# Optimization experiments

Measured on AMD Instinct MI355X. Metric: run time of the kernel, lower is better.

## Reference

```python
import jax, jax.numpy as jnp
import numpy as np

N, L, D = 32768, 15, 256
VOCAB, SCORE_MAX = 27, 100


def setup_inputs() -> dict:
    key = jax.random.key(0)
    ks = jax.random.split(key, 16)
    inp = {
        'words': jax.random.randint(ks[0], (N, L), 0, VOCAB, dtype=jnp.int32),
        'rows': jax.random.randint(ks[1], (N,), 0, L, dtype=jnp.int32),
        'cols': jax.random.randint(ks[2], (N,), 0, L, dtype=jnp.int32),
        'dirs': jax.random.randint(ks[3], (N,), 0, 2, dtype=jnp.int32),
        'scores': jax.random.randint(ks[4], (N,), 0, 150, dtype=jnp.int32),
        'letter_emb': jax.random.normal(ks[5], (VOCAB, D), jnp.float32),
        'positional': jax.random.normal(ks[6], (L, D), jnp.float32),
        'Wq': jax.random.normal(ks[7], (D, D), jnp.float32) / np.sqrt(D),
        'bq': jax.random.normal(ks[8], (D,), jnp.float32) * 0.01,
        'Wk': jax.random.normal(ks[9], (D, D), jnp.float32) / np.sqrt(D),
        'bk': jax.random.normal(ks[10], (D,), jnp.float32) * 0.01,
        'Wv': jax.random.normal(ks[11], (D, D), jnp.float32) / np.sqrt(D),
        'bv': jax.random.normal(ks[12], (D,), jnp.float32) * 0.01,
        'row_emb': jax.random.normal(ks[13], (L, D), jnp.float32),
        'col_emb': jax.random.normal(ks[14], (L, D), jnp.float32),
        'dir_emb': jax.random.normal(ks[15], (2, D), jnp.float32),
        'score_emb': jax.random.normal(jax.random.fold_in(key, 99), (SCORE_MAX, D), jnp.float32),
    }
    return inp


def reference(words, rows, cols, dirs, scores, letter_emb, positional, Wq, bq, Wk, bk, Wv, bv, row_emb, col_emb, dir_emb, score_emb):
    # WordEncoder: letter embedding + positional, then single-head self-attention, sum over positions
    emb = letter_emb[words] + positional[None, :, :]            # [N, L, D]
    q = emb @ Wq.T + bq                                          # [N, L, D]
    k = emb @ Wk.T + bk
    v = emb @ Wv.T + bv
    att = jax.nn.softmax(jnp.einsum('nld,nmd->nlm', q, k), axis=-1)  # [N, L, L]
    word = jnp.einsum('nlm,nmd->nd', att, v)                     # (att @ v).sum(axis=1) -> [N, D]
    # VectorEncoder
    vector = row_emb[rows] + col_emb[cols] + dir_emb[dirs]       # [N, D]
    # score embedding (clamped to score_max - 1)
    score_v = score_emb[jnp.minimum(scores, SCORE_MAX - 1)]      # [N, D]
    # original computes word_enc(move.word) twice (word + ordered) -> 2 * word
    return 2.0 * word + vector + score_v
```

## Files before the change

### kernel.cpp

```cpp
#include <hip/hip_runtime.h>
#include <hip/hip_bf16.h>

#define NMOV 32768
#define LW 15
#define DIM 256
#define NVOC 27
#define NR 405
#define GSH 408
#define MPB 8

__device__ __forceinline__ float b2f(unsigned short u) {
    return __uint_as_float(((unsigned int)u) << 16);
}

__device__ const unsigned char PAIR_LUT[120] = {
    0x00,
    0x10,0x11,
    0x20,0x21,0x22,
    0x30,0x31,0x32,0x33,
    0x40,0x41,0x42,0x43,0x44,
    0x50,0x51,0x52,0x53,0x54,0x55,
    0x60,0x61,0x62,0x63,0x64,0x65,0x66,
    0x70,0x71,0x72,0x73,0x74,0x75,0x76,0x77,
    0x80,0x81,0x82,0x83,0x84,0x85,0x86,0x87,0x88,
    0x90,0x91,0x92,0x93,0x94,0x95,0x96,0x97,0x98,0x99,
    0xA0,0xA1,0xA2,0xA3,0xA4,0xA5,0xA6,0xA7,0xA8,0xA9,0xAA,
    0xB0,0xB1,0xB2,0xB3,0xB4,0xB5,0xB6,0xB7,0xB8,0xB9,0xBA,0xBB,
    0xC0,0xC1,0xC2,0xC3,0xC4,0xC5,0xC6,0xC7,0xC8,0xC9,0xCA,0xCB,0xCC,
    0xD0,0xD1,0xD2,0xD3,0xD4,0xD5,0xD6,0xD7,0xD8,0xD9,0xDA,0xDB,0xDC,0xDD,
    0xE0,0xE1,0xE2,0xE3,0xE4,0xE5,0xE6,0xE7,0xE8,0xE9,0xEA,0xEB,0xEC,0xED,0xEE
};

__global__ __launch_bounds__(256) void qkv_tables(
    const float* __restrict__ le, const float* __restrict__ pos,
    const float* __restrict__ Wq, const float* __restrict__ bq,
    const float* __restrict__ Wk, const float* __restrict__ bk,
    const float* __restrict__ Wv, const float* __restrict__ bv,
    float* __restrict__ QT, float* __restrict__ KT,
    __hip_bfloat16* __restrict__ VT)
{
    const int b   = blockIdx.x;
    const int c   = b / 15;
    const int rem = b % 15;
    const int lg  = rem / 3;
    const int mat = rem % 3;
    const int d   = threadIdx.x;

    const float* W  = (mat == 0) ? Wq : (mat == 1) ? Wk : Wv;
    const float* bb = (mat == 0) ? bq : (mat == 1) ? bk : bv;

    __shared__ float e[3][DIM];
    const float lv = le[c * DIM + d];
    #pragma unroll
    for (int k = 0; k < 3; ++k)
        e[k][d] = lv + pos[(lg * 3 + k) * DIM + d];
    __syncthreads();

    float acc[3];
    const float bias = bb[d];
    #pragma unroll
    for (int k = 0; k < 3; ++k) acc[k] = bias;

    const float4* w4 = (const float4*)(W + d * DIM);
    #pragma unroll 8
    for (int j4 = 0; j4 < DIM / 4; ++j4) {
        float4 w = w4[j4];
        #pragma unroll
        for (int k = 0; k < 3; ++k) {
            float4 e4 = *(const float4*)&e[k][j4 * 4];
            acc[k] += e4.x * w.x + e4.y * w.y + e4.z * w.z + e4.w * w.w;
        }
    }
    #pragma unroll
    for (int k = 0; k < 3; ++k) {
        int r = c * LW + lg * 3 + k;
        if (mat == 0)      QT[r * DIM + d] = acc[k];
        else if (mat == 1) KT[r * DIM + d] = acc[k];
        else               VT[r * DIM + d] = __float2bfloat16(acc[k]);
    }
}

__global__ __launch_bounds__(256) void h_matrix(
    const float* __restrict__ QT, const float* __restrict__ KT,
    float2* __restrict__ H)
{
    __shared__ float Qi[16][68], Ki[16][68], Qj[16][68], Kj[16][68];

    int rem = blockIdx.x, bi = 0, cnt = 26;
    while (rem >= cnt) { rem -= cnt; ++bi; --cnt; }
    const int bj = bi + rem;
    const int i0 = bi * 16, j0 = bj * 16;
    const int t = threadIdx.x;
    const int ti = t >> 4, tj = t & 15;

    float acc_ij = 0.f, acc_ji = 0.f;

    for (int k0 = 0; k0 < DIM; k0 += 64) {
        #pragma unroll
        for (int s = 0; s < 4; ++s) {
            int slot = s * 256 + t;
            int tile = slot >> 8;
            int r    = (slot >> 4) & 15;
            int c4   = slot & 15;
            int grow = (tile < 2) ? (i0 + r) : (j0 + r);
            const float* src = (tile == 0 || tile == 2) ? QT : KT;
            float4 v = (grow < NR)
                ? *(const float4*)&src[grow * DIM + k0 + c4 * 4]
                : make_float4(0.f, 0.f, 0.f, 0.f);
            float* dst = (tile == 0) ? &Qi[r][c4 * 4]
                       : (tile == 1) ? &Ki[r][c4 * 4]
                       : (tile == 2) ? &Qj[r][c4 * 4] : &Kj[r][c4 * 4];
            *(float4*)dst = v;
        }
        __syncthreads();
        #pragma unroll 4
        for (int k = 0; k < 64; k += 4) {
            float4 qi = *(const float4*)&Qi[ti][k];
            float4 kj = *(const float4*)&Kj[tj][k];
            float4 qj = *(const float4*)&Qj[ti][k];
            float4 ki = *(const float4*)&Ki[tj][k];
            acc_ij += qi.x * kj.x + qi.y * kj.y + qi.z * kj.z + qi.w * kj.w;
            acc_ji += qj.x * ki.x + qj.y * ki.y + qj.z * ki.z + qj.w * ki.w;
        }
        __syncthreads();
    }

    Qi[ti][tj] = acc_ij;
    Ki[ti][tj] = acc_ji;
    __syncthreads();
    const float t_ij = Qi[tj][ti];
    const float t_ji = Ki[tj][ti];

    const int i1 = i0 + ti, j1 = j0 + tj;
    if (i1 < NR && j1 < NR) H[i1 * GSH + j1] = make_float2(acc_ij, t_ji);
    const int i2 = j0 + ti, j2 = i0 + tj;
    if (i2 < NR && j2 < NR) H[i2 * GSH + j2] = make_float2(acc_ji, t_ij);
}

__global__ __launch_bounds__(256) void moves_kernel(
    const int* __restrict__ words, const int* __restrict__ rowsI,
    const int* __restrict__ colsI, const int* __restrict__ dirsI,
    const int* __restrict__ scoresI,
    const float2* __restrict__ H, const __hip_bfloat16* __restrict__ VT,
    const float* __restrict__ row_emb, const float* __restrict__ col_emb,
    const float* __restrict__ dir_emb, const float* __restrict__ score_emb,
    float* __restrict__ out)
{
    __shared__ float S[MPB][LW][17];
    __shared__ int   rIdx[MPB][16];
    __shared__ float csum[MPB][16];
    const int base = blockIdx.x * MPB;
    const int t = threadIdx.x;
    const int mv = t >> 5;
    const int j  = t & 31;

    if (j < LW)
        rIdx[mv][j] = words[(base + mv) * LW + j] * LW + j;
    __builtin_amdgcn_wave_barrier();

    #pragma unroll
    for (int k = 0; k < 4; ++k) {
        int p = j + 32 * k;
        if (p < 120) {
            int lm = PAIR_LUT[p];
            int l = lm >> 4, m = lm & 15;
            int rl = rIdx[mv][l], rm = rIdx[mv][m];
            float2 hv = H[(size_t)rl * GSH + rm];
            S[mv][l][m] = hv.x;
            S[mv][m][l] = hv.y;
        }
    }
    __builtin_amdgcn_wave_barrier();

    if (j < LW) {
        float s[LW];
        #pragma unroll
        for (int m = 0; m < LW; ++m) s[m] = S[mv][j][m];
        float mx = s[0];
        #pragma unroll
        for (int m = 1; m < LW; ++m) mx = fmaxf(mx, s[m]);
        float sum = 0.f;
        #pragma unroll
        for (int m = 0; m < LW; ++m) { s[m] = __expf(s[m] - mx); sum += s[m]; }
        float inv = 1.0f / sum;
        #pragma unroll
        for (int m = 0; m < LW; ++m) S[mv][j][m] = s[m] * inv;
    }
    __builtin_amdgcn_wave_barrier();

    if (j < LW) {
        float acc = 0.f;
        #pragma unroll
        for (int l = 0; l < LW; ++l) acc += S[mv][l][j];
        csum[mv][j] = acc;
    }
    __builtin_amdgcn_wave_barrier();

    const int wv = t >> 6;
    const int d0 = (t & 63) * 4;
    #pragma unroll
    for (int s2 = 0; s2 < 2; ++s2) {
        const int i = wv * 2 + s2;
        const int n = base + i;
        float wx = 0.f, wy = 0.f, wz = 0.f, ww = 0.f;
        #pragma unroll
        for (int m = 0; m < LW; ++m) {
            float c = csum[i][m];
            int r = rIdx[i][m];
            ushort4 vv = *(const ushort4*)((const unsigned short*)VT + (size_t)r * DIM + d0);
            wx += c * b2f(vv.x); wy += c * b2f(vv.y);
            wz += c * b2f(vv.z); ww += c * b2f(vv.w);
        }
        float4 re = *(const float4*)&row_emb[rowsI[n] * DIM + d0];
        float4 ce = *(const float4*)&col_emb[colsI[n] * DIM + d0];
        float4 de = *(const float4*)&dir_emb[dirsI[n] * DIM + d0];
        float4 se = *(const float4*)&score_emb[min(scoresI[n], 99) * DIM + d0];
        float4 res;
        res.x = 2.f * wx + re.x + ce.x + de.x + se.x;
        res.y = 2.f * wy + re.y + ce.y + de.y + se.y;
        res.z = 2.f * wz + re.z + ce.z + de.z + se.z;
        res.w = 2.f * ww + re.w + ce.w + de.w + se.w;
        *(float4*)&out[(size_t)n * DIM + d0] = res;
    }
}

extern "C" void kernel_launch(void* const* d_in, const int* in_sizes, int n_in,
                              void* d_out, int out_size, void* d_ws, size_t ws_size,
                              hipStream_t stream)
{
    const int*   words      = (const int*)d_in[0];
    const int*   rowsI      = (const int*)d_in[1];
    const int*   colsI      = (const int*)d_in[2];
    const int*   dirsI      = (const int*)d_in[3];
    const int*   scoresI    = (const int*)d_in[4];
    const float* letter_emb = (const float*)d_in[5];
    const float* positional = (const float*)d_in[6];
    const float* Wq         = (const float*)d_in[7];
    const float* bq         = (const float*)d_in[8];
    const float* Wk         = (const float*)d_in[9];
    const float* bk         = (const float*)d_in[10];
    const float* Wv         = (const float*)d_in[11];
    const float* bv         = (const float*)d_in[12];
    const float* row_emb    = (const float*)d_in[13];
    const float* col_emb    = (const float*)d_in[14];
    const float* dir_emb    = (const float*)d_in[15];
    const float* score_emb  = (const float*)d_in[16];
    float* out = (float*)d_out;

    float*  QT = (float*)d_ws;
    float*  KT = QT + NR * DIM;
    float2* Hm = (float2*)(KT + NR * DIM);
    __hip_bfloat16* VT = (__hip_bfloat16*)((char*)Hm + (size_t)NR * GSH * sizeof(float2));

    qkv_tables<<<405, 256, 0, stream>>>(letter_emb, positional, Wq, bq, Wk, bk,
                                        Wv, bv, QT, KT, VT);
    h_matrix<<<351, 256, 0, stream>>>(QT, KT, Hm);
    moves_kernel<<<NMOV / MPB, 256, 0, stream>>>(words, rowsI, colsI, dirsI,
                                                 scoresI, Hm, VT, row_emb,
                                                 col_emb, dir_emb, score_emb,
                                                 out);
}
```

Measured before the change: 68.65 us.

## Tile QKV table GEMM in shared memory and prefetch V rows in moves kernel

```diff
diff --git a/kernel.cpp b/kernel.cpp
--- a/kernel.cpp
+++ b/kernel.cpp
@@ -31,7 +31,7 @@
     0xE0,0xE1,0xE2,0xE3,0xE4,0xE5,0xE6,0xE7,0xE8,0xE9,0xEA,0xEB,0xEC,0xED,0xEE
 };
 
-__global__ __launch_bounds__(256) void qkv_tables(
+__global__ __launch_bounds__(256) void qkv_gemm(
     const float* __restrict__ le, const float* __restrict__ pos,
     const float* __restrict__ Wq, const float* __restrict__ bq,
     const float* __restrict__ Wk, const float* __restrict__ bk,
@@ -39,44 +39,74 @@
     float* __restrict__ QT, float* __restrict__ KT,
     __hip_bfloat16* __restrict__ VT)
 {
-    const int b   = blockIdx.x;
-    const int c   = b / 15;
-    const int rem = b % 15;
-    const int lg  = rem / 3;
-    const int mat = rem % 3;
-    const int d   = threadIdx.x;
-
+    __shared__ float Ash[32][260];
+    __shared__ float Bsh[256][69];
+    const int t  = threadIdx.x;
+    const int gx = blockIdx.x % 12;
+    const int gy = blockIdx.x / 12;
+    const int r0 = gy * 32;
+    const int mat = gx >> 2;
+    const int nb  = (gx & 3) * 64;
     const float* W  = (mat == 0) ? Wq : (mat == 1) ? Wk : Wv;
     const float* bb = (mat == 0) ? bq : (mat == 1) ? bk : bv;
 
-    __shared__ float e[3][DIM];
-    const float lv = le[c * DIM + d];
-    #pragma unroll
-    for (int k = 0; k < 3; ++k)
-        e[k][d] = lv + pos[(lg * 3 + k) * DIM + d];
+    #pragma unroll
+    for (int s = 0; s < 8; ++s) {
+        int slot = s * 256 + t;
+        int row = slot >> 6, q4 = slot & 63;
+        int r = r0 + row;
+        float4 v = make_float4(0.f, 0.f, 0.f, 0.f);
+        if (r < NR) {
+            int c = r / 15, l = r - c * 15;
+            float4 lv = *(const float4*)&le[c * DIM + q4 * 4];
+            float4 pv = *(const float4*)&pos[l * DIM + q4 * 4];
+            v = make_float4(lv.x + pv.x, lv.y + pv.y, lv.z + pv.z, lv.w + pv.w);
+        }
+        *(float4*)&Ash[row][q4 * 4] = v;
+    }
+    #pragma unroll
+    for (int s = 0; s < 16; ++s) {
+        int slot = s * 256 + t;
+        int row = slot >> 6, q4 = slot & 63;
+        float4 w4 = *(const float4*)&W[(nb + row) * DIM + q4 * 4];
+        Bsh[q4 * 4 + 0][row] = w4.x;
+        Bsh[q4 * 4 + 1][row] = w4.y;
+        Bsh[q4 * 4 + 2][row] = w4.z;
+        Bsh[q4 * 4 + 3][row] = w4.w;
+    }
     __syncthreads();
 
-    float acc[3];
-    const float bias = bb[d];
-    #pragma unroll
-    for (int k = 0; k < 3; ++k) acc[k] = bias;
-
-    const float4* w4 = (const float4*)(W + d * DIM);
-    #pragma unroll 8
-    for (int j4 = 0; j4 < DIM / 4; ++j4) {
-        float4 w = w4[j4];
-        #pragma unroll
-        for (int k = 0; k < 3; ++k) {
-            float4 e4 = *(const float4*)&e[k][j4 * 4];
-            acc[k] += e4.x * w.x + e4.y * w.y + e4.z * w.z + e4.w * w.w;
-        }
-    }
-    #pragma unroll
-    for (int k = 0; k < 3; ++k) {
-        int r = c * LW + lg * 3 + k;
-        if (mat == 0)      QT[r * DIM + d] = acc[k];
-        else if (mat == 1) KT[r * DIM + d] = acc[k];
-        else               VT[r * DIM + d] = __float2bfloat16(acc[k]);
+    const int tn = t & 63, tm = t >> 6;
+    float acc[8];
+    #pragma unroll
+    for (int rr = 0; rr < 8; ++rr) acc[rr] = 0.f;
+
+    #pragma unroll 4
+    for (int kq = 0; kq < 64; ++kq) {
+        float4 a4[8];
+        #pragma unroll
+        for (int rr = 0; rr < 8; ++rr)
+            a4[rr] = *(const float4*)&Ash[tm * 8 + rr][kq * 4];
+        float b0 = Bsh[kq * 4 + 0][tn];
+        float b1 = Bsh[kq * 4 + 1][tn];
+        float b2 = Bsh[kq * 4 + 2][tn];
+        float b3 = Bsh[kq * 4 + 3][tn];
+        #pragma unroll
+        for (int rr = 0; rr < 8; ++rr)
+            acc[rr] += a4[rr].x * b0 + a4[rr].y * b1 + a4[rr].z * b2 + a4[rr].w * b3;
+    }
+
+    const float bias = bb[nb + tn];
+    const int dcol = nb + tn;
+    #pragma unroll
+    for (int rr = 0; rr < 8; ++rr) {
+        int r = r0 + tm * 8 + rr;
+        if (r < NR) {
+            float v = acc[rr] + bias;
+            if (mat == 0)      QT[r * DIM + dcol] = v;
+            else if (mat == 1) KT[r * DIM + dcol] = v;
+            else               VT[r * DIM + dcol] = __float2bfloat16(v);
+        }
     }
 }
 
@@ -158,16 +188,41 @@
         rIdx[mv][j] = words[(base + mv) * LW + j] * LW + j;
     __builtin_amdgcn_wave_barrier();
 
+    const int wv = t >> 6;
+    const int d0 = (t & 63) * 4;
+    const unsigned short* VT16 = (const unsigned short*)VT;
+
+    float2 hv[4];
+    int ll[4], mm[4];
     #pragma unroll
     for (int k = 0; k < 4; ++k) {
         int p = j + 32 * k;
         if (p < 120) {
             int lm = PAIR_LUT[p];
-            int l = lm >> 4, m = lm & 15;
-            int rl = rIdx[mv][l], rm = rIdx[mv][m];
-            float2 hv = H[(size_t)rl * GSH + rm];
-            S[mv][l][m] = hv.x;
-            S[mv][m][l] = hv.y;
+            ll[k] = lm >> 4; mm[k] = lm & 15;
+            int rl = rIdx[mv][ll[k]], rm = rIdx[mv][mm[k]];
+            hv[k] = H[(size_t)rl * GSH + rm];
+        }
+    }
+
+    const int iA = wv * 2, nA = base + iA;
+    ushort4 vvA[LW];
+    #pragma unroll
+    for (int m = 0; m < LW; ++m) {
+        int r = rIdx[iA][m];
+        vvA[m] = *(const ushort4*)(VT16 + (size_t)r * DIM + d0);
+    }
+    float4 reA = *(const float4*)&row_emb[rowsI[nA] * DIM + d0];
+    float4 ceA = *(const float4*)&col_emb[colsI[nA] * DIM + d0];
+    float4 deA = *(const float4*)&dir_emb[dirsI[nA] * DIM + d0];
+    float4 seA = *(const float4*)&score_emb[min(scoresI[nA], 99) * DIM + d0];
+
+    #pragma unroll
+    for (int k = 0; k < 4; ++k) {
+        int p = j + 32 * k;
+        if (p < 120) {
+            S[mv][ll[k]][mm[k]] = hv[k].x;
+            S[mv][mm[k]][ll[k]] = hv[k].y;
         }
     }
     __builtin_amdgcn_wave_barrier();
@@ -196,31 +251,48 @@
     }
     __builtin_amdgcn_wave_barrier();
 
-    const int wv = t >> 6;
-    const int d0 = (t & 63) * 4;
-    #pragma unroll
-    for (int s2 = 0; s2 < 2; ++s2) {
-        const int i = wv * 2 + s2;
-        const int n = base + i;
+    {
         float wx = 0.f, wy = 0.f, wz = 0.f, ww = 0.f;
         #pragma unroll
         for (int m = 0; m < LW; ++m) {
-            float c = csum[i][m];
-            int r = rIdx[i][m];
-            ushort4 vv = *(const ushort4*)((const unsigned short*)VT + (size_t)r * DIM + d0);
-            wx += c * b2f(vv.x); wy += c * b2f(vv.y);
-            wz += c * b2f(vv.z); ww += c * b2f(vv.w);
-        }
-        float4 re = *(const float4*)&row_emb[rowsI[n] * DIM + d0];
-        float4 ce = *(const float4*)&col_emb[colsI[n] * DIM + d0];
-        float4 de = *(const float4*)&dir_emb[dirsI[n] * DIM + d0];
-        float4 se = *(const float4*)&score_emb[min(scoresI[n], 99) * DIM + d0];
+            float c = csum[iA][m];
+            wx += c * b2f(vvA[m].x); wy += c * b2f(vvA[m].y);
+            wz += c * b2f(vvA[m].z); ww += c * b2f(vvA[m].w);
+        }
         float4 res;
-        res.x = 2.f * wx + re.x + ce.x + de.x + se.x;
-        res.y = 2.f * wy + re.y + ce.y + de.y + se.y;
-        res.z = 2.f * wz + re.z + ce.z + de.z + se.z;
-        res.w = 2.f * ww + re.w + ce.w + de.w + se.w;
-        *(float4*)&out[(size_t)n * DIM + d0] = res;
+        res.x = 2.f * wx + reA.x + ceA.x + deA.x + seA.x;
+        res.y = 2.f * wy + reA.y + ceA.y + deA.y + seA.y;
+        res.z = 2.f * wz + reA.z + ceA.z + deA.z + seA.z;
+        res.w = 2.f * ww + reA.w + ceA.w + deA.w + seA.w;
+        *(float4*)&out[(size_t)nA * DIM + d0] = res;
+    }
+
+    {
+        const int iB = wv * 2 + 1, nB = base + iB;
+        ushort4 vvB[LW];
+        #pragma unroll
+        for (int m = 0; m < LW; ++m) {
+            int r = rIdx[iB][m];
+            vvB[m] = *(const ushort4*)(VT16 + (size_t)r * DIM + d0);
+        }
+        float4 reB = *(const float4*)&row_emb[rowsI[nB] * DIM + d0];
+        float4 ceB = *(const float4*)&col_emb[colsI[nB] * DIM + d0];
+        float4 deB = *(const float4*)&dir_emb[dirsI[nB] * DIM + d0];
+        float4 seB = *(const float4*)&score_emb[min(scoresI[nB], 99) * DIM + d0];
+
+        float wx = 0.f, wy = 0.f, wz = 0.f, ww = 0.f;
+        #pragma unroll
+        for (int m = 0; m < LW; ++m) {
+            float c = csum[iB][m];
+            wx += c * b2f(vvB[m].x); wy += c * b2f(vvB[m].y);
+            wz += c * b2f(vvB[m].z); ww += c * b2f(vvB[m].w);
+        }
+        float4 res;
+        res.x = 2.f * wx + reB.x + ceB.x + deB.x + seB.x;
+        res.y = 2.f * wy + reB.y + ceB.y + deB.y + seB.y;
+        res.z = 2.f * wz + reB.z + ceB.z + deB.z + seB.z;
+        res.w = 2.f * ww + reB.w + ceB.w + deB.w + seB.w;
+        *(float4*)&out[(size_t)nB * DIM + d0] = res;
     }
 }
 
@@ -252,8 +324,8 @@
     float2* Hm = (float2*)(KT + NR * DIM);
     __hip_bfloat16* VT = (__hip_bfloat16*)((char*)Hm + (size_t)NR * GSH * sizeof(float2));
 
-    qkv_tables<<<405, 256, 0, stream>>>(letter_emb, positional, Wq, bq, Wk, bk,
-                                        Wv, bv, QT, KT, VT);
+    qkv_gemm<<<156, 256, 0, stream>>>(letter_emb, positional, Wq, bq, Wk, bk,
+                                      Wv, bv, QT, KT, VT);
     h_matrix<<<351, 256, 0, stream>>>(QT, KT, Hm);
     moves_kernel<<<NMOV / MPB, 256, 0, stream>>>(words, rowsI, colsI, dirsI,
                                                  scoresI, Hm, VT, row_emb,
```

Result: no change. 68.01 us (-0.9%).
